# Optimization experiments

Hardware: AMD Instinct MI355X
Metric: run time of the kernel (lower is better)

Reference implementation:

```python
import jax, jax.numpy as jnp
import numpy as np

N, IN_DIM, OUT_DIM = 4096, 512, 512
H, D = 8, OUT_DIM // 8          # num_heads, head_dim
ALPHA = 0.2                     # leaky relu slope
NEG = -9e15
EPS = 1e-5


def setup_inputs() -> dict:
    key = jax.random.key(0)
    k1, k2, k3, k4 = jax.random.split(key, 4)
    x = jax.random.normal(k1, (N, IN_DIM), dtype=jnp.float32)
    adj = jax.random.randint(k2, (N, N), 0, 2, dtype=jnp.int32)
    # scale params like nn.Linear default init (~1/sqrt(fan_in)) to keep scores sane
    W = jax.random.normal(k3, (OUT_DIM, IN_DIM), dtype=jnp.float32) / np.sqrt(IN_DIM)
    a = jax.random.normal(k4, (2 * D,), dtype=jnp.float32) / np.sqrt(2 * D)
    gamma = jnp.ones((OUT_DIM,), dtype=jnp.float32)
    beta = jnp.zeros((OUT_DIM,), dtype=jnp.float32)
    return {"x": x, "adj": adj, "W": W, "a": a, "gamma": gamma, "beta": beta}


def reference(x, adj, W, a, gamma, beta):
    n = x.shape[0]
    Wh = (x @ W.T).reshape(n, H, D)                       # [N, H, D]
    a_src, a_dst = a[:D], a[D:]                           # shared across heads
    s_src = jnp.einsum('jhd,d->jh', Wh, a_src)            # [N, H] source term
    s_dst = jnp.einsum('ihd,d->ih', Wh, a_dst)            # [N, H] dest term
    # e[i, j, h] = leakyrelu(a_src . Wh[j,h] + a_dst . Wh[i,h]); row i = dst, col j = src
    e = jax.nn.leaky_relu(s_dst[:, None, :] + s_src[None, :, :], negative_slope=ALPHA)
    e = jnp.where((adj > 0)[:, :, None], e, NEG)          # mask non-edges
    attn = jax.nn.softmax(e, axis=1)                      # softmax over source nodes j
    h_prime = jnp.einsum('ijh,jhd->ihd', attn, Wh).reshape(n, H * D)  # [N, out_dim]
    # BatchNorm1d (training-mode batch statistics, biased variance)
    mean = jnp.mean(h_prime, axis=0)
    var = jnp.var(h_prime, axis=0)
    h_prime = gamma * (h_prime - mean) * jax.lax.rsqrt(var + EPS) + beta
    return jax.nn.relu(h_prime)
```

## Files before the change

kernel.cpp:

```cpp
#include <hip/hip_runtime.h>
#include <hip/hip_bf16.h>
#include <hip/hip_fp16.h>
#include <stdint.h>


typedef __attribute__((ext_vector_type(4))) float f32x4;
typedef __attribute__((ext_vector_type(8))) short s16x8;
typedef __attribute__((ext_vector_type(2))) _Float16 h2v;

#define LOG2E 1.4426950408889634f

static __device__ __forceinline__ ushort f2bf(float f) {
  union { float f; uint32_t u; } v; v.f = f;
  uint32_t r = (v.u + 0x7FFFu + ((v.u >> 16) & 1u)) >> 16;
  return (ushort)r;
}

static __device__ __forceinline__ short bf16b(float f) {
  __hip_bfloat16 h = __float2bfloat16(f);
  union { __hip_bfloat16 h; short s; } c; c.h = h;
  return c.s;
}

static __device__ __forceinline__ float bf2f(ushort u) {
  union { uint32_t u; float f; } c; c.u = ((uint32_t)u) << 16;
  return c.f;
}

static __device__ __forceinline__ ushort hbits(float f) {
  union { _Float16 h; ushort u; } c; c.h = (_Float16)f;
  return c.u;
}

static __device__ __forceinline__ h2v u2h2(uint32_t u) {
  union { uint32_t u; h2v h; } c; c.u = u; return c.h;
}
static __device__ __forceinline__ uint32_t h22u(h2v h) {
  union { uint32_t u; h2v h; } c; c.h = h; return c.u;
}

static __device__ __forceinline__ void gl_lds16(const ushort* g, ushort* l) {
  __builtin_amdgcn_global_load_lds(
      (const __attribute__((address_space(1))) unsigned int*)(g),
      (__attribute__((address_space(3))) unsigned int*)(l), 16, 0, 0);
}

__global__ __launch_bounds__(256) void k_prep(const float* __restrict__ x,
                                              const float* __restrict__ W,
                                              const int* __restrict__ adj,
                                              ushort* __restrict__ xb,
                                              ushort* __restrict__ wb,
                                              unsigned long long* __restrict__ maskw,
                                              float* __restrict__ stats) {
  const int t = threadIdx.x;
  if (blockIdx.x < 2304) {
    const int idx = (blockIdx.x * 256 + t) * 4;
    const int NX = 4096 * 512;
    if (idx < NX) {
      float4 v = *(const float4*)(x + idx);
      ushort4 o; o.x = f2bf(v.x); o.y = f2bf(v.y); o.z = f2bf(v.z); o.w = f2bf(v.w);
      *(ushort4*)(xb + idx) = o;
    } else {
      const int k = idx - NX;
      float4 v = *(const float4*)(W + k);
      ushort4 o; o.x = f2bf(v.x); o.y = f2bf(v.y); o.z = f2bf(v.z); o.w = f2bf(v.w);
      *(ushort4*)(wb + k) = o;
    }
  } else {
    const int pb = blockIdx.x - 2304;
    if (pb == 0) {
      stats[t] = 0.f; stats[t + 256] = 0.f; stats[t + 512] = 0.f; stats[t + 768] = 0.f;
    }
    const size_t base = (size_t)pb * 8192;
    const int lane = t & 63;
#pragma unroll 4
    for (int it = 0; it < 32; ++it) {
      const size_t elem = base + it * 256 + t;
      unsigned long long b = __ballot(adj[elem] > 0);
      if (lane == 0) maskw[elem >> 6] = b;
    }
  }
}

__global__ __launch_bounds__(256) void k_gemm(const ushort* __restrict__ xb,
                                              const ushort* __restrict__ wb,
                                              const float* __restrict__ a,
                                              ushort* __restrict__ WhT,
                                              ushort* __restrict__ EsT,
                                              ushort* __restrict__ es2T,
                                              float* __restrict__ rT) {
  __shared__ ushort bt[64 * 512];
  float* tl = (float*)bt;
  const int lane = threadIdx.x & 63;
  const int wv = threadIdx.x >> 6;
  const int l15 = lane & 15, lg = lane >> 4;
  const int m0 = blockIdx.x * 64;
  const int h = blockIdx.y;
  const int n0 = h * 64;

#pragma unroll
  for (int it = 0; it < 16; ++it) {
    const int col = it * 4 + wv;
    const ushort* src = wb + (size_t)(n0 + col) * 512 + (lane ^ (col & 7)) * 8;
    gl_lds16(src, &bt[col * 512]);
  }
  __syncthreads();

  const ushort* ap = xb + (size_t)(m0 + wv * 16 + l15) * 512 + lg * 8;
  f32x4 acc[4] = {};
  for (int k0 = 0; k0 < 512; k0 += 32) {
    s16x8 av = *(const s16x8*)(ap + k0);
#pragma unroll
    for (int ct = 0; ct < 4; ++ct) {
      const int col = ct * 16 + l15;
      s16x8 b = *(const s16x8*)((const char*)bt + col * 1024 +
                                (((k0 + lg * 8) * 2) ^ ((col & 7) << 4)));
      acc[ct] = __builtin_amdgcn_mfma_f32_16x16x32_bf16(av, b, acc[ct], 0, 0, 0);
    }
  }
  float aS[4], aD[4];
#pragma unroll
  for (int ct = 0; ct < 4; ++ct) {
    aS[ct] = a[ct * 16 + l15];
    aD[ct] = a[64 + ct * 16 + l15];
  }
#pragma unroll
  for (int r = 0; r < 4; ++r) {
    float s1 = acc[0][r] * aS[0] + acc[1][r] * aS[1] + acc[2][r] * aS[2] + acc[3][r] * aS[3];
    float s2 = acc[0][r] * aD[0] + acc[1][r] * aD[1] + acc[2][r] * aD[2] + acc[3][r] * aD[3];
#pragma unroll
    for (int off = 1; off < 16; off <<= 1) {
      s1 += __shfl_xor(s1, off);
      s2 += __shfl_xor(s2, off);
    }
    if (l15 == 0) {
      const int row = m0 + wv * 16 + lg * 4 + r;
      const float aa = s1 * LOG2E;
      const float bb = s2 * LOG2E;
      EsT[h * 4096 + row]  = hbits(__builtin_amdgcn_exp2f(aa));
      es2T[h * 4096 + row] = hbits(__builtin_amdgcn_exp2f(0.2f * aa));
      rT[h * 4096 + row]   = __builtin_amdgcn_exp2f(-0.8f * bb);
    }
  }
  __syncthreads();
#pragma unroll
  for (int ct = 0; ct < 4; ++ct)
#pragma unroll
    for (int r = 0; r < 4; ++r)
      tl[(ct * 16 + l15) * 65 + wv * 16 + lg * 4 + r] = acc[ct][r];
  __syncthreads();
  const int c = threadIdx.x >> 2, mb = (threadIdx.x & 3) * 16;
  s16x8 o0, o1;
#pragma unroll
  for (int k = 0; k < 8; ++k) o0[k] = (short)hbits(tl[c * 65 + mb + k]);
#pragma unroll
  for (int k = 0; k < 8; ++k) o1[k] = (short)hbits(tl[c * 65 + mb + 8 + k]);
  *(s16x8*)(WhT + (size_t)(n0 + c) * 4096 + m0 + mb) = o0;
  *(s16x8*)(WhT + (size_t)(n0 + c) * 4096 + m0 + mb + 8) = o1;
}

__global__ __launch_bounds__(512, 4) void k_attn(
    const uint32_t* __restrict__ mask32,
    const ushort* __restrict__ WhT,
    const ushort* __restrict__ EsT,
    const ushort* __restrict__ es2T,
    const float* __restrict__ rT,
    ushort* __restrict__ num,
    float* __restrict__ lbuf) {
  __shared__ ushort tile[4][4096];
  __shared__ uint32_t mask_s[256 * 33];
  __shared__ uint32_t Es_s[512];
  __shared__ uint32_t es2_s[512];

  const int t = threadIdx.x;
  const int lane = t & 63, wv = t >> 6;
  const int l15 = lane & 15, lg = lane >> 4;
  const int h = blockIdx.y;
  const int jh = blockIdx.x & 3;
  const int ih = blockIdx.x >> 2;
  const int i0b = ih * 256;
  const int j0 = jh * 1024;

  if (t < 128) {
    ((uint4*)Es_s)[t] = ((const uint4*)EsT)[(h * 4096 + j0) / 8 + t];
  } else if (t < 256) {
    ((uint4*)es2_s)[t - 128] = ((const uint4*)es2T)[(h * 4096 + j0) / 8 + t - 128];
  }
  {
    const int r = t >> 1, part = t & 1;
    const uint32_t* src = mask32 + (size_t)(i0b + r) * 128 + jh * 32 + part * 16;
    uint32_t* dst = &mask_s[r * 33 + part * 16];
#pragma unroll
    for (int k = 0; k < 4; ++k)
      *(int4*)(dst + k * 4) = *(const int4*)(src + k * 4);
  }
  const int cg = (wv << 3) + (lane >> 3);
  const int gg = (lane & 7) ^ (cg & 7);
  const ushort* sbase = WhT + (size_t)(h * 64 + cg) * 4096 + j0 + gg * 8;

  gl_lds16(sbase, &tile[0][wv * 512]);
  gl_lds16(sbase + 64, &tile[1][wv * 512]);
  gl_lds16(sbase + 128, &tile[2][wv * 512]);
  __syncthreads();

  const int rloc = wv * 32 + l15;
  const float r0f = rT[h * 4096 + i0b + rloc];
  const float r1f = rT[h * 4096 + i0b + rloc + 16];
  const h2v r02 = {(_Float16)r0f, (_Float16)r0f};
  const h2v r12 = {(_Float16)r1f, (_Float16)r1f};

  f32x4 acc[2][4] = {};
  f32x4 accd0 = {}, accd1 = {};
  s16x8 bones;
  {
    const short v = (l15 == 0) ? (short)0x3C00 : (short)0;
    bones[0] = v; bones[1] = v; bones[2] = v; bones[3] = v;
    bones[4] = v; bones[5] = v; bones[6] = v; bones[7] = v;
  }

#pragma unroll 1
  for (int c = 0; c < 16; ++c) {
    if (c < 14)       asm volatile("s_waitcnt vmcnt(2)" ::: "memory");
    else if (c == 14) asm volatile("s_waitcnt vmcnt(1)" ::: "memory");
    else              asm volatile("s_waitcnt vmcnt(0)" ::: "memory");
    __builtin_amdgcn_s_barrier();
    if (c < 13) gl_lds16(sbase + (size_t)(c + 3) * 64, &tile[(c + 3) & 3][wv * 512]);
    const char* tb = (const char*)&tile[c & 3][0];
#pragma unroll
    for (int half = 0; half < 2; ++half) {
      const int jsub = half * 32;
      const uint4 e4 = *(const uint4*)&Es_s[c * 32 + (jsub >> 1) + lg * 4];
      const uint4 f4 = *(const uint4*)&es2_s[c * 32 + (jsub >> 1) + lg * 4];
      const uint32_t w0 = mask_s[rloc * 33 + c * 2 + half] >> (lg * 8);
      const uint32_t w1 = mask_s[(rloc + 16) * 33 + c * 2 + half] >> (lg * 8);
      s16x8 b[4];
#pragma unroll
      for (int ct = 0; ct < 4; ++ct) {
        const int col = ct * 16 + l15;
        b[ct] = *(const s16x8*)(tb + col * 128 + ((jsub * 2 + lg * 16) ^ ((col & 7) << 4)));
      }
      union { s16x8 v8; uint32_t u32[4]; } pa0, pa1;
#pragma unroll
      for (int q2 = 0; q2 < 4; ++q2) {
        const int q = q2 * 2;
        const h2v e2 = u2h2(((const uint32_t*)&e4)[q2]);
        const h2v f2 = u2h2(((const uint32_t*)&f4)[q2]);
        const h2v t0 = __builtin_elementwise_max(e2, r02 * f2);
        const h2v t1 = __builtin_elementwise_max(e2, r12 * f2);
        const uint32_t mk0 = (((w0 >> q) & 1u) | (((w0 >> q) & 2u) << 15)) * 0xFFFFu;
        const uint32_t mk1 = (((w1 >> q) & 1u) | (((w1 >> q) & 2u) << 15)) * 0xFFFFu;
        pa0.u32[q2] = mk0 & h22u(t0);
        pa1.u32[q2] = mk1 & h22u(t1);
      }
      accd0 = __builtin_amdgcn_mfma_f32_16x16x32_f16(pa0.v8, bones, accd0, 0, 0, 0);
      accd1 = __builtin_amdgcn_mfma_f32_16x16x32_f16(pa1.v8, bones, accd1, 0, 0, 0);
#pragma unroll
      for (int ct = 0; ct < 4; ++ct) {
        acc[0][ct] = __builtin_amdgcn_mfma_f32_16x16x32_f16(pa0.v8, b[ct], acc[0][ct], 0, 0, 0);
        acc[1][ct] = __builtin_amdgcn_mfma_f32_16x16x32_f16(pa1.v8, b[ct], acc[1][ct], 0, 0, 0);
      }
    }
  }

  if (l15 == 0) {
    float* lb = &lbuf[((size_t)jh * 8 + h) * 4096 + i0b + rloc];
#pragma unroll
    for (int r = 0; r < 4; ++r) lb[lg * 4 + r] = accd0[r];
#pragma unroll
    for (int r = 0; r < 4; ++r) lb[16 + lg * 4 + r] = accd1[r];
  }
  ushort* np = num + (size_t)jh * 4096 * 512;
#pragma unroll
  for (int rs = 0; rs < 2; ++rs)
#pragma unroll
    for (int ct = 0; ct < 4; ++ct)
#pragma unroll
      for (int r = 0; r < 4; ++r)
        np[(size_t)(i0b + wv * 32 + rs * 16 + lg * 4 + r) * 512 + h * 64 + ct * 16 + l15] =
            (ushort)bf16b(acc[rs][ct][r]);
}

__global__ __launch_bounds__(512) void k_stats(const ushort* __restrict__ num,
                                               const float* __restrict__ lbuf,
                                               ushort* __restrict__ hpb,
                                               float* __restrict__ stats) {
  __shared__ float linv_s[128];
  const int t = threadIdx.x;
  const int r0 = blockIdx.x * 16;
  if (t < 128) {
    const int r = r0 + (t >> 3), hh = t & 7;
    float l = 0.f;
#pragma unroll
    for (int s = 0; s < 4; ++s) l += lbuf[((size_t)s * 8 + hh) * 4096 + r];
    linv_s[t] = 1.0f / l;
  }
  __syncthreads();
  const int c = t;
  const int hh = c >> 6;
  float s1 = 0.f, s2 = 0.f;
  for (int rr = 0; rr < 16; ++rr) {
    const int r = r0 + rr;
    float nsum = 0.f;
#pragma unroll
    for (int s = 0; s < 4; ++s)
      nsum += bf2f(num[(size_t)s * 4096 * 512 + (size_t)r * 512 + c]);
    const float v = nsum * linv_s[rr * 8 + hh];
    hpb[(size_t)r * 512 + c] = (ushort)bf16b(v);
    s1 += v; s2 += v * v;
  }
  atomicAdd(&stats[c], s1);
  atomicAdd(&stats[512 + c], s2);
}

__global__ __launch_bounds__(256) void k_apply(const ushort* __restrict__ hpb,
                                               const float* __restrict__ stats,
                                               const float* __restrict__ gamma,
                                               const float* __restrict__ beta,
                                               float* __restrict__ out) {
  const size_t idx8 = ((size_t)blockIdx.x * 256 + threadIdx.x) * 8;
  const int c0 = (int)(idx8 & 511);
  s16x8 hv = *(const s16x8*)(hpb + idx8);
#pragma unroll
  for (int k = 0; k < 8; ++k) {
    const int cc = c0 + k;
    const float mean = stats[cc] * (1.f / 4096.f);
    const float var = stats[512 + cc] * (1.f / 4096.f) - mean * mean;
    const float v = bf2f((ushort)hv[k]);
    const float val = (v - mean) * rsqrtf(var + 1e-5f) * gamma[cc] + beta[cc];
    out[idx8 + k] = fmaxf(val, 0.f);
  }
}

extern "C" void kernel_launch(void* const* d_in, const int* in_sizes, int n_in,
                              void* d_out, int out_size, void* d_ws, size_t ws_size,
                              hipStream_t stream) {
  const float* x = (const float*)d_in[0];
  const int* adj = (const int*)d_in[1];
  const float* W = (const float*)d_in[2];
  const float* a = (const float*)d_in[3];
  const float* gamma = (const float*)d_in[4];
  const float* beta = (const float*)d_in[5];
  float* out = (float*)d_out;

  char* ws = (char*)d_ws;
  size_t off = 0;
  auto alloc = [&](size_t bytes) -> void* {
    void* p = ws + off;
    off += (bytes + 255) & ~(size_t)255;
    return p;
  };
  ushort* WhT   = (ushort*)alloc((size_t)512 * 4096 * 2);
  ushort* EsT   = (ushort*)alloc((size_t)8 * 4096 * 2);
  ushort* es2T  = (ushort*)alloc((size_t)8 * 4096 * 2);
  float*  rT    = (float*)alloc((size_t)8 * 4096 * 4);
  unsigned long long* maskw = (unsigned long long*)alloc((size_t)4096 * 64 * 8);
  float*  lbuf  = (float*)alloc((size_t)32 * 4096 * 4);
  ushort* hpb   = (ushort*)alloc((size_t)4096 * 512 * 2);
  float*  stats = (float*)alloc((size_t)1024 * 4);
  const size_t ov = off;
  ushort* xb = (ushort*)(ws + ov);
  ushort* wb = (ushort*)(ws + ov + (size_t)4096 * 512 * 2);
  ushort* num = (ushort*)(ws + ov);

  hipLaunchKernelGGL(k_prep, dim3(4352), dim3(256), 0, stream,
                     x, W, adj, xb, wb, maskw, stats);
  hipLaunchKernelGGL(k_gemm, dim3(64, 8), dim3(256), 0, stream, xb, wb, a,
                     WhT, EsT, es2T, rT);
  hipLaunchKernelGGL(k_attn, dim3(64, 8), dim3(512), 0, stream,
                     (const uint32_t*)maskw, WhT, EsT, es2T, rT, num, lbuf);
  hipLaunchKernelGGL(k_stats, dim3(256), dim3(512), 0, stream, num, lbuf, hpb, stats);
  hipLaunchKernelGGL(k_apply, dim3(1024), dim3(256), 0, stream, hpb, stats, gamma, beta, out);
}
```

Before: 75.20 us.

## Fuse bf16 conversion and GEMM into mask-building kernel, drop prep pass

```diff
diff --git a/kernel.cpp b/kernel.cpp
--- a/kernel.cpp
+++ b/kernel.cpp
@@ -10,12 +10,6 @@
 
 #define LOG2E 1.4426950408889634f
 
-static __device__ __forceinline__ ushort f2bf(float f) {
-  union { float f; uint32_t u; } v; v.f = f;
-  uint32_t r = (v.u + 0x7FFFu + ((v.u >> 16) & 1u)) >> 16;
-  return (ushort)r;
-}
-
 static __device__ __forceinline__ short bf16b(float f) {
   __hip_bfloat16 h = __float2bfloat16(f);
   union { __hip_bfloat16 h; short s; } c; c.h = h;
@@ -45,29 +39,19 @@
       (__attribute__((address_space(3))) unsigned int*)(l), 16, 0, 0);
 }
 
-__global__ __launch_bounds__(256) void k_prep(const float* __restrict__ x,
+__global__ __launch_bounds__(256) void k_main(const float* __restrict__ x,
                                               const float* __restrict__ W,
                                               const int* __restrict__ adj,
-                                              ushort* __restrict__ xb,
-                                              ushort* __restrict__ wb,
+                                              const float* __restrict__ a,
                                               unsigned long long* __restrict__ maskw,
-                                              float* __restrict__ stats) {
+                                              float* __restrict__ stats,
+                                              ushort* __restrict__ WhT,
+                                              ushort* __restrict__ EsT,
+                                              ushort* __restrict__ es2T,
+                                              float* __restrict__ rT) {
   const int t = threadIdx.x;
-  if (blockIdx.x < 2304) {
-    const int idx = (blockIdx.x * 256 + t) * 4;
-    const int NX = 4096 * 512;
-    if (idx < NX) {
-      float4 v = *(const float4*)(x + idx);
-      ushort4 o; o.x = f2bf(v.x); o.y = f2bf(v.y); o.z = f2bf(v.z); o.w = f2bf(v.w);
-      *(ushort4*)(xb + idx) = o;
-    } else {
-      const int k = idx - NX;
-      float4 v = *(const float4*)(W + k);
-      ushort4 o; o.x = f2bf(v.x); o.y = f2bf(v.y); o.z = f2bf(v.z); o.w = f2bf(v.w);
-      *(ushort4*)(wb + k) = o;
-    }
-  } else {
-    const int pb = blockIdx.x - 2304;
+  if (blockIdx.x < 2048) {
+    const int pb = blockIdx.x;
     if (pb == 0) {
       stats[t] = 0.f; stats[t + 256] = 0.f; stats[t + 512] = 0.f; stats[t + 768] = 0.f;
     }
@@ -79,43 +63,34 @@
       unsigned long long b = __ballot(adj[elem] > 0);
       if (lane == 0) maskw[elem >> 6] = b;
     }
-  }
-}
-
-__global__ __launch_bounds__(256) void k_gemm(const ushort* __restrict__ xb,
-                                              const ushort* __restrict__ wb,
-                                              const float* __restrict__ a,
-                                              ushort* __restrict__ WhT,
-                                              ushort* __restrict__ EsT,
-                                              ushort* __restrict__ es2T,
-                                              float* __restrict__ rT) {
-  __shared__ ushort bt[64 * 512];
-  float* tl = (float*)bt;
-  const int lane = threadIdx.x & 63;
-  const int wv = threadIdx.x >> 6;
+    return;
+  }
+  __shared__ float tl[64 * 65];
+  const int g = blockIdx.x - 2048;
+  const int lane = t & 63;
+  const int wv = t >> 6;
   const int l15 = lane & 15, lg = lane >> 4;
-  const int m0 = blockIdx.x * 64;
-  const int h = blockIdx.y;
+  const int m0 = (g & 63) * 64;
+  const int h = g >> 6;
   const int n0 = h * 64;
 
-#pragma unroll
-  for (int it = 0; it < 16; ++it) {
-    const int col = it * 4 + wv;
-    const ushort* src = wb + (size_t)(n0 + col) * 512 + (lane ^ (col & 7)) * 8;
-    gl_lds16(src, &bt[col * 512]);
-  }
-  __syncthreads();
-
-  const ushort* ap = xb + (size_t)(m0 + wv * 16 + l15) * 512 + lg * 8;
+  const float* apf = x + (size_t)(m0 + wv * 16 + l15) * 512 + lg * 8;
   f32x4 acc[4] = {};
   for (int k0 = 0; k0 < 512; k0 += 32) {
-    s16x8 av = *(const s16x8*)(ap + k0);
+    float4 a0 = *(const float4*)(apf + k0);
+    float4 a1 = *(const float4*)(apf + k0 + 4);
+    s16x8 av;
+    av[0] = bf16b(a0.x); av[1] = bf16b(a0.y); av[2] = bf16b(a0.z); av[3] = bf16b(a0.w);
+    av[4] = bf16b(a1.x); av[5] = bf16b(a1.y); av[6] = bf16b(a1.z); av[7] = bf16b(a1.w);
 #pragma unroll
     for (int ct = 0; ct < 4; ++ct) {
-      const int col = ct * 16 + l15;
-      s16x8 b = *(const s16x8*)((const char*)bt + col * 1024 +
-                                (((k0 + lg * 8) * 2) ^ ((col & 7) << 4)));
-      acc[ct] = __builtin_amdgcn_mfma_f32_16x16x32_bf16(av, b, acc[ct], 0, 0, 0);
+      const float* bpf = W + (size_t)(n0 + ct * 16 + l15) * 512 + k0 + lg * 8;
+      float4 b0 = *(const float4*)(bpf);
+      float4 b1 = *(const float4*)(bpf + 4);
+      s16x8 bv;
+      bv[0] = bf16b(b0.x); bv[1] = bf16b(b0.y); bv[2] = bf16b(b0.z); bv[3] = bf16b(b0.w);
+      bv[4] = bf16b(b1.x); bv[5] = bf16b(b1.y); bv[6] = bf16b(b1.z); bv[7] = bf16b(b1.w);
+      acc[ct] = __builtin_amdgcn_mfma_f32_16x16x32_bf16(av, bv, acc[ct], 0, 0, 0);
     }
   }
   float aS[4], aD[4];
@@ -142,14 +117,13 @@
       rT[h * 4096 + row]   = __builtin_amdgcn_exp2f(-0.8f * bb);
     }
   }
-  __syncthreads();
 #pragma unroll
   for (int ct = 0; ct < 4; ++ct)
 #pragma unroll
     for (int r = 0; r < 4; ++r)
       tl[(ct * 16 + l15) * 65 + wv * 16 + lg * 4 + r] = acc[ct][r];
   __syncthreads();
-  const int c = threadIdx.x >> 2, mb = (threadIdx.x & 3) * 16;
+  const int c = t >> 2, mb = (t & 3) * 16;
   s16x8 o0, o1;
 #pragma unroll
   for (int k = 0; k < 8; ++k) o0[k] = (short)hbits(tl[c * 65 + mb + k]);
@@ -357,15 +331,10 @@
   float*  lbuf  = (float*)alloc((size_t)32 * 4096 * 4);
   ushort* hpb   = (ushort*)alloc((size_t)4096 * 512 * 2);
   float*  stats = (float*)alloc((size_t)1024 * 4);
-  const size_t ov = off;
-  ushort* xb = (ushort*)(ws + ov);
-  ushort* wb = (ushort*)(ws + ov + (size_t)4096 * 512 * 2);
-  ushort* num = (ushort*)(ws + ov);
-
-  hipLaunchKernelGGL(k_prep, dim3(4352), dim3(256), 0, stream,
-                     x, W, adj, xb, wb, maskw, stats);
-  hipLaunchKernelGGL(k_gemm, dim3(64, 8), dim3(256), 0, stream, xb, wb, a,
-                     WhT, EsT, es2T, rT);
+  ushort* num   = (ushort*)alloc((size_t)4 * 4096 * 512 * 2);
+
+  hipLaunchKernelGGL(k_main, dim3(2560), dim3(256), 0, stream,
+                     x, W, adj, a, maskw, stats, WhT, EsT, es2T, rT);
   hipLaunchKernelGGL(k_attn, dim3(64, 8), dim3(512), 0, stream,
                      (const uint32_t*)maskw, WhT, EsT, es2T, rT, num, lbuf);
   hipLaunchKernelGGL(k_stats, dim3(256), dim3(512), 0, stream, num, lbuf, hpb, stats);
```

Result: slower. 149.9 us (+99.3%).
